# Optimization experiments

Measured on AMD Instinct MI355X. Metric: run time of the kernel, lower is better.

Reference implementation:

```python
import jax, jax.numpy as jnp
import numpy as np

B, N, D = 512, 16384, 2  # batch of weight vectors, grid points, 2-D geometry


def _eig_power(eigs, q, p):
    # reconstruct Q diag(eigs**p) Q^T ; eigs [B,D], q [B,D,D]
    return (q * (eigs ** p)[..., None, :]) @ jnp.swapaxes(q, -1, -2)


def _make_gauss(geo, w):
    # geo [N,D], w [B,N] (rows sum to 1)
    mean = w @ geo                               # [B,D]
    centered = geo[None, :, :] - mean[:, None, :]  # [B,N,D]
    denom = 1.0 - jnp.sum(w * w, axis=-1)        # [B] reliability-weight correction
    cov = jnp.einsum('bn,bnd,bne->bde', w, centered, centered) / denom[:, None, None]
    return mean, cov, centered


def setup_inputs() -> dict:
    key = jax.random.key(0)
    k1, k2, k3, k4 = jax.random.split(key, 4)
    geo_x = jax.random.uniform(k1, (N, D), dtype=jnp.float32)
    geo_y = jax.random.uniform(k2, (N, D), dtype=jnp.float32)
    a = jax.random.uniform(k3, (B, N), dtype=jnp.float32, minval=0.1, maxval=1.0)
    a = a / jnp.sum(a, axis=-1, keepdims=True)
    b = jax.random.uniform(k4, (B, N), dtype=jnp.float32, minval=0.1, maxval=1.0)
    b = b / jnp.sum(b, axis=-1, keepdims=True)
    return {"geo_x": geo_x, "geo_y": geo_y, "a": a, "b": b}


def reference(geo_x, geo_y, a, b):
    mean_a, cov_a, cx = _make_gauss(geo_x, a)   # cov_a [B,D,D], cx [B,N,D]
    mean_b, cov_b, _ = _make_gauss(geo_y, b)
    # Gaussian OT map: sigma0^{-1/2} (sigma0^{1/2} sigma1 sigma0^{1/2})^{1/2} sigma0^{-1/2}
    e0, q0 = jnp.linalg.eigh(cov_a)
    sqrt0 = _eig_power(e0, q0, 0.5)
    sqrt0_inv = _eig_power(e0, q0, -0.5)
    mid = sqrt0 @ cov_b @ sqrt0
    e1, q1 = jnp.linalg.eigh(mid)
    m = _eig_power(e1, q1, 0.5)
    a2b = sqrt0_inv @ m @ sqrt0_inv             # [B,D,D]
    # quadratic form (centered_x * (A2B centered_x^T)^T).sum(-1)
    quad = jnp.einsum('bnd,bde,bne->bn', cx, a2b, cx)  # [B,N]
    f = 2.0 * (0.5 * jnp.sum(geo_x * geo_x, axis=1)[None, :]
               - 0.5 * quad
               - mean_b @ geo_x.T)
    f = f - jnp.mean(f, axis=1, keepdims=True)
    return f
```

## Files before the change

### kernel.cpp

```cpp
#include <hip/hip_runtime.h>

static constexpr int TPB = 256;
static constexpr int NSLICE = 4;

using f4 = __attribute__((ext_vector_type(4))) float;

__device__ __forceinline__ float wave_reduce_f32(float v) {
#pragma unroll
    for (int off = 32; off > 0; off >>= 1)
        v += __shfl_down(v, off, 64);
    return v;
}

__global__ __launch_bounds__(TPB) void kstats(const float* __restrict__ gx,
                                              const float* __restrict__ gy,
                                              const float* __restrict__ a,
                                              const float* __restrict__ bw,
                                              int N, int B,
                                              double* __restrict__ spart,
                                              double* __restrict__ gpart) {
    const int s = blockIdx.x;
    const int b = blockIdx.y;
    const int n4   = N / 4;
    const int per  = n4 / NSLICE;
    const int base = s * per;
    const f4* gx4 = reinterpret_cast<const f4*>(gx);
    const int lane = threadIdx.x & 63, wid = threadIdx.x >> 6;

    if (b == B) {
        float sx = 0, sy = 0, sxx = 0, sxy = 0, syy = 0;
        for (int i = base + threadIdx.x; i < base + per; i += TPB) {
            f4 g0 = gx4[2 * i], g1 = gx4[2 * i + 1];
            float x0 = g0[0], y0 = g0[1], x1 = g0[2], y1 = g0[3];
            float x2 = g1[0], y2 = g1[1], x3 = g1[2], y3 = g1[3];
            sx  += (x0 + x1) + (x2 + x3);
            sy  += (y0 + y1) + (y2 + y3);
            sxx += x0 * x0 + x1 * x1 + x2 * x2 + x3 * x3;
            sxy += x0 * y0 + x1 * y1 + x2 * y2 + x3 * y3;
            syy += y0 * y0 + y1 * y1 + y2 * y2 + y3 * y3;
        }
        float accg[5] = {sx, sy, sxx, sxy, syy};
        __shared__ double redg[4][5];
#pragma unroll
        for (int k = 0; k < 5; k++) {
            float v = wave_reduce_f32(accg[k]);
            if (lane == 0) redg[wid][k] = (double)v;
        }
        __syncthreads();
        if (threadIdx.x < 5)
            gpart[s * 5 + threadIdx.x] = redg[0][threadIdx.x] + redg[1][threadIdx.x] +
                                         redg[2][threadIdx.x] + redg[3][threadIdx.x];
        return;
    }

    const f4* a4  = reinterpret_cast<const f4*>(a  + (size_t)b * N);
    const f4* b4  = reinterpret_cast<const f4*>(bw + (size_t)b * N);
    const f4* gy4 = reinterpret_cast<const f4*>(gy);

    float acc[12];
#pragma unroll
    for (int k = 0; k < 12; k++) acc[k] = 0.0f;

    const int i0 = base + threadIdx.x;

#pragma unroll
    for (int half = 0; half < 2; half++) {
        const int ia = i0 + (2 * half) * TPB;
        const int ib = i0 + (2 * half + 1) * TPB;
        f4 av0 = a4[ia],  av1 = a4[ib];
        f4 bv0 = b4[ia],  bv1 = b4[ib];
        f4 gA0 = gx4[2 * ia], gA1 = gx4[2 * ia + 1];
        f4 gB0 = gx4[2 * ib], gB1 = gx4[2 * ib + 1];
        f4 hA0 = gy4[2 * ia], hA1 = gy4[2 * ia + 1];
        f4 hB0 = gy4[2 * ib], hB1 = gy4[2 * ib + 1];

#pragma unroll
        for (int q = 0; q < 2; q++) {
            f4 av = q ? av1 : av0;
            f4 bv = q ? bv1 : bv0;
            f4 g0 = q ? gB0 : gA0, g1 = q ? gB1 : gA1;
            f4 h0 = q ? hB0 : hA0, h1 = q ? hB1 : hA1;
            float wa[4] = {av[0], av[1], av[2], av[3]};
            float wb[4] = {bv[0], bv[1], bv[2], bv[3]};
            float px[4] = {g0[0], g0[2], g1[0], g1[2]};
            float py[4] = {g0[1], g0[3], g1[1], g1[3]};
            float qx[4] = {h0[0], h0[2], h1[0], h1[2]};
            float qy[4] = {h0[1], h0[3], h1[1], h1[3]};
#pragma unroll
            for (int j = 0; j < 4; j++) {
                float w = wa[j], x = px[j], y = py[j];
                float wx = w * x, wy = w * y;
                acc[0] += wx;
                acc[1] += wy;
                acc[2] += wx * x;
                acc[3] += wx * y;
                acc[4] += wy * y;
                acc[5] += w * w;
                float v = wb[j], u = qx[j], t = qy[j];
                float vu = v * u, vt = v * t;
                acc[6]  += vu;
                acc[7]  += vt;
                acc[8]  += vu * u;
                acc[9]  += vu * t;
                acc[10] += vt * t;
                acc[11] += v * v;
            }
        }
    }

    __shared__ double red[4][12];
#pragma unroll
    for (int k = 0; k < 12; k++) {
        float v = wave_reduce_f32(acc[k]);
        if (lane == 0) red[wid][k] = (double)v;
    }
    __syncthreads();
    if (threadIdx.x < 12) {
        spart[((size_t)b * NSLICE + s) * 12 + threadIdx.x] =
            red[0][threadIdx.x] + red[1][threadIdx.x] +
            red[2][threadIdx.x] + red[3][threadIdx.x];
    }
}

__global__ __launch_bounds__(TPB) void kemit(const float* __restrict__ gx,
                                             const double* __restrict__ spart,
                                             const double* __restrict__ gpart,
                                             int N, float* __restrict__ out) {
    const int b = blockIdx.y;
    __shared__ double sh12[12];
    __shared__ double shg[5];
    __shared__ float shc[10];

    const f4* gx4 = reinterpret_cast<const f4*>(gx);
    const int i0 = blockIdx.x * (TPB * 4) + threadIdx.x;
    f4 g[8];
#pragma unroll
    for (int k = 0; k < 4; k++) {
        g[2 * k]     = gx4[2 * (i0 + k * TPB)];
        g[2 * k + 1] = gx4[2 * (i0 + k * TPB) + 1];
    }

    if (threadIdx.x < 12) {
        double t = 0;
#pragma unroll
        for (int s = 0; s < NSLICE; s++)
            t += spart[((size_t)b * NSLICE + s) * 12 + threadIdx.x];
        sh12[threadIdx.x] = t;
    } else if (threadIdx.x >= 64 && threadIdx.x < 69) {
        double t = 0;
#pragma unroll
        for (int s = 0; s < NSLICE; s++) t += gpart[s * 5 + (threadIdx.x - 64)];
        shg[threadIdx.x - 64] = t / (double)N;
    }
    __syncthreads();

    if (threadIdx.x == 0) {
        double mx  = sh12[0],  my  = sh12[1],  Saxx = sh12[2],  Saxy = sh12[3],  Sayy = sh12[4],  Saa = sh12[5];
        double mbx = sh12[6],  mby = sh12[7],  Sbxx = sh12[8],  Sbxy = sh12[9],  Sbyy = sh12[10], Sbb = sh12[11];

        double da = 1.0 - Saa, db = 1.0 - Sbb;
        double Caxx = (Saxx - mx * mx) / da;
        double Caxy = (Saxy - mx * my) / da;
        double Cayy = (Sayy - my * my) / da;
        double Cbxx = (Sbxx - mbx * mbx) / db;
        double Cbxy = (Sbxy - mbx * mby) / db;
        double Cbyy = (Sbyy - mby * mby) / db;

        double s0 = sqrt(fmax(Caxx * Cayy - Caxy * Caxy, 0.0));
        double t0 = sqrt(Caxx + Cayy + 2.0 * s0);
        double Rxx = (Caxx + s0) / t0, Rxy = Caxy / t0, Ryy = (Cayy + s0) / t0;
        double detR = Rxx * Ryy - Rxy * Rxy;
        double Ixx = Ryy / detR, Ixy = -Rxy / detR, Iyy = Rxx / detR;

        double Txx = Cbxx * Rxx + Cbxy * Rxy;
        double Txy = Cbxx * Rxy + Cbxy * Ryy;
        double Tyx = Cbxy * Rxx + Cbyy * Rxy;
        double Tyy = Cbxy * Rxy + Cbyy * Ryy;
        double midxx = Rxx * Txx + Rxy * Tyx;
        double midyy = Rxy * Txy + Ryy * Tyy;
        double midxy = 0.5 * ((Rxx * Txy + Rxy * Tyy) + (Rxy * Txx + Ryy * Tyx));

        double s1 = sqrt(fmax(midxx * midyy - midxy * midxy, 0.0));
        double t1 = sqrt(midxx + midyy + 2.0 * s1);
        double Mxx = (midxx + s1) / t1, Mxy = midxy / t1, Myy = (midyy + s1) / t1;

        double Uxx = Mxx * Ixx + Mxy * Ixy;
        double Uxy = Mxx * Ixy + Mxy * Iyy;
        double Uyx = Mxy * Ixx + Myy * Ixy;
        double Uyy = Mxy * Ixy + Myy * Iyy;
        double Axx = Ixx * Uxx + Ixy * Uyx;
        double Axy = Ixx * Uxy + Ixy * Uyy;
        double Ayy = Ixy * Uxy + Iyy * Uyy;

        shc[0] = (float)(1.0 - Axx);
        shc[1] = (float)(1.0 - Ayy);
        shc[2] = (float)(-2.0 * Axy);
        shc[3] = (float)(2.0 * (Axx * mx + Axy * my - mbx));
        shc[4] = (float)(2.0 * (Ayy * my + Axy * mx - mby));
        shc[5] = (float)shg[0];
        shc[6] = (float)shg[1];
        shc[7] = (float)shg[2];
        shc[8] = (float)shg[3];
        shc[9] = (float)shg[4];
    }
    __syncthreads();

    const float cxx = shc[0], cyy = shc[1], cxy = shc[2], cx = shc[3], cy = shc[4];
    const float Ex = shc[5], Ey = shc[6], Ex2 = shc[7], Exy = shc[8], Ey2 = shc[9];

    f4* out4 = reinterpret_cast<f4*>(out + (size_t)b * N);
#pragma unroll
    for (int k = 0; k < 4; k++) {
        int i = i0 + k * TPB;
        f4 g0 = g[2 * k], g1 = g[2 * k + 1];
        float rx[4] = {g0[0], g0[2], g1[0], g1[2]};
        float ry[4] = {g0[1], g0[3], g1[1], g1[3]};
        f4 o;
#pragma unroll
        for (int j = 0; j < 4; j++) {
            float x = rx[j], y = ry[j];
            o[j] = cxx * (x * x - Ex2) + cyy * (y * y - Ey2) + cxy * (x * y - Exy) +
                   cx * (x - Ex) + cy * (y - Ey);
        }
        __builtin_nontemporal_store(o, out4 + i);
    }
}

extern "C" void kernel_launch(void* const* d_in, const int* in_sizes, int n_in,
                              void* d_out, int out_size, void* d_ws, size_t ws_size,
                              hipStream_t stream) {
    const float* geo_x = (const float*)d_in[0];
    const float* geo_y = (const float*)d_in[1];
    const float* a     = (const float*)d_in[2];
    const float* b     = (const float*)d_in[3];
    float* out = (float*)d_out;

    int N = in_sizes[0] / 2;
    int B = in_sizes[2] / N;

    char* ws = (char*)d_ws;
    double* gpart = (double*)ws;
    double* spart = (double*)(ws + 512);

    kstats<<<dim3(NSLICE, B + 1), TPB, 0, stream>>>(geo_x, geo_y, a, b, N, B,
                                                    spart, gpart);
    kemit<<<dim3((N / 4) / (TPB * 4), B), TPB, 0, stream>>>(geo_x, spart, gpart, N, out);
}
```

Measured before the change: 26.14 us.

## Batch eight rows per emit block and fold mean-centering into a constant

The emit kernel now has each block handle eight batch rows over a smaller point slice. It loads the geometry once and reuses it for every row, and eight threads compute the per-row 2x2 OT coefficients in parallel instead of one. The mean-subtraction terms are folded into a single constant K, so the per-point polynomial becomes a short FMA chain. The stats kernel also issues all four loads up front instead of two at a time. Fewer blocks and more work per block cut redundant geometry reads and serial setup, but reduce grid parallelism and assume B is divisible by eight.

Result: slower. 27.21 us (+4.1%).

```diff
diff --git a/kernel.cpp b/kernel.cpp
--- a/kernel.cpp
+++ b/kernel.cpp
@@ -2,6 +2,8 @@
 
 static constexpr int TPB = 256;
 static constexpr int NSLICE = 4;
+static constexpr int ROWB = 8;
+static constexpr int PF = 2;
 
 using f4 = __attribute__((ext_vector_type(4))) float;
 
@@ -62,49 +64,44 @@
     for (int k = 0; k < 12; k++) acc[k] = 0.0f;
 
     const int i0 = base + threadIdx.x;
-
-#pragma unroll
-    for (int half = 0; half < 2; half++) {
-        const int ia = i0 + (2 * half) * TPB;
-        const int ib = i0 + (2 * half + 1) * TPB;
-        f4 av0 = a4[ia],  av1 = a4[ib];
-        f4 bv0 = b4[ia],  bv1 = b4[ib];
-        f4 gA0 = gx4[2 * ia], gA1 = gx4[2 * ia + 1];
-        f4 gB0 = gx4[2 * ib], gB1 = gx4[2 * ib + 1];
-        f4 hA0 = gy4[2 * ia], hA1 = gy4[2 * ia + 1];
-        f4 hB0 = gy4[2 * ib], hB1 = gy4[2 * ib + 1];
-
-#pragma unroll
-        for (int q = 0; q < 2; q++) {
-            f4 av = q ? av1 : av0;
-            f4 bv = q ? bv1 : bv0;
-            f4 g0 = q ? gB0 : gA0, g1 = q ? gB1 : gA1;
-            f4 h0 = q ? hB0 : hA0, h1 = q ? hB1 : hA1;
-            float wa[4] = {av[0], av[1], av[2], av[3]};
-            float wb[4] = {bv[0], bv[1], bv[2], bv[3]};
-            float px[4] = {g0[0], g0[2], g1[0], g1[2]};
-            float py[4] = {g0[1], g0[3], g1[1], g1[3]};
-            float qx[4] = {h0[0], h0[2], h1[0], h1[2]};
-            float qy[4] = {h0[1], h0[3], h1[1], h1[3]};
-#pragma unroll
-            for (int j = 0; j < 4; j++) {
-                float w = wa[j], x = px[j], y = py[j];
-                float wx = w * x, wy = w * y;
-                acc[0] += wx;
-                acc[1] += wy;
-                acc[2] += wx * x;
-                acc[3] += wx * y;
-                acc[4] += wy * y;
-                acc[5] += w * w;
-                float v = wb[j], u = qx[j], t = qy[j];
-                float vu = v * u, vt = v * t;
-                acc[6]  += vu;
-                acc[7]  += vt;
-                acc[8]  += vu * u;
-                acc[9]  += vu * t;
-                acc[10] += vt * t;
-                acc[11] += v * v;
-            }
+    f4 av[4], bv[4], gA[4], gB[4], hA[4], hB[4];
+#pragma unroll
+    for (int q = 0; q < 4; q++) {
+        const int i = i0 + q * TPB;
+        av[q] = a4[i];
+        bv[q] = b4[i];
+        gA[q] = gx4[2 * i];
+        gB[q] = gx4[2 * i + 1];
+        hA[q] = gy4[2 * i];
+        hB[q] = gy4[2 * i + 1];
+    }
+
+#pragma unroll
+    for (int q = 0; q < 4; q++) {
+        float wa[4] = {av[q][0], av[q][1], av[q][2], av[q][3]};
+        float wb[4] = {bv[q][0], bv[q][1], bv[q][2], bv[q][3]};
+        float px[4] = {gA[q][0], gA[q][2], gB[q][0], gB[q][2]};
+        float py[4] = {gA[q][1], gA[q][3], gB[q][1], gB[q][3]};
+        float qx[4] = {hA[q][0], hA[q][2], hB[q][0], hB[q][2]};
+        float qy[4] = {hA[q][1], hA[q][3], hB[q][1], hB[q][3]};
+#pragma unroll
+        for (int j = 0; j < 4; j++) {
+            float w = wa[j], x = px[j], y = py[j];
+            float wx = w * x, wy = w * y;
+            acc[0] += wx;
+            acc[1] += wy;
+            acc[2] += wx * x;
+            acc[3] += wx * y;
+            acc[4] += wy * y;
+            acc[5] += w * w;
+            float v = wb[j], u = qx[j], t = qy[j];
+            float vu = v * u, vt = v * t;
+            acc[6]  += vu;
+            acc[7]  += vt;
+            acc[8]  += vu * u;
+            acc[9]  += vu * t;
+            acc[10] += vt * t;
+            acc[11] += v * v;
         }
     }
 
@@ -126,37 +123,40 @@
                                              const double* __restrict__ spart,
                                              const double* __restrict__ gpart,
                                              int N, float* __restrict__ out) {
-    const int b = blockIdx.y;
-    __shared__ double sh12[12];
-    __shared__ double shg[5];
-    __shared__ float shc[10];
+    const int b0 = blockIdx.y * ROWB;
+    __shared__ float shc[ROWB][8];
 
     const f4* gx4 = reinterpret_cast<const f4*>(gx);
-    const int i0 = blockIdx.x * (TPB * 4) + threadIdx.x;
-    f4 g[8];
-#pragma unroll
-    for (int k = 0; k < 4; k++) {
+    const int i0 = blockIdx.x * (TPB * PF) + threadIdx.x;
+    f4 g[2 * PF];
+#pragma unroll
+    for (int k = 0; k < PF; k++) {
         g[2 * k]     = gx4[2 * (i0 + k * TPB)];
         g[2 * k + 1] = gx4[2 * (i0 + k * TPB) + 1];
     }
 
-    if (threadIdx.x < 12) {
-        double t = 0;
-#pragma unroll
-        for (int s = 0; s < NSLICE; s++)
-            t += spart[((size_t)b * NSLICE + s) * 12 + threadIdx.x];
-        sh12[threadIdx.x] = t;
-    } else if (threadIdx.x >= 64 && threadIdx.x < 69) {
-        double t = 0;
-#pragma unroll
-        for (int s = 0; s < NSLICE; s++) t += gpart[s * 5 + (threadIdx.x - 64)];
-        shg[threadIdx.x - 64] = t / (double)N;
-    }
-    __syncthreads();
-
-    if (threadIdx.x == 0) {
-        double mx  = sh12[0],  my  = sh12[1],  Saxx = sh12[2],  Saxy = sh12[3],  Sayy = sh12[4],  Saa = sh12[5];
-        double mbx = sh12[6],  mby = sh12[7],  Sbxx = sh12[8],  Sbxy = sh12[9],  Sbyy = sh12[10], Sbb = sh12[11];
+    if (threadIdx.x < ROWB) {
+        const int r = b0 + threadIdx.x;
+        double s12[12];
+#pragma unroll
+        for (int k = 0; k < 12; k++) {
+            double t = 0;
+#pragma unroll
+            for (int s = 0; s < NSLICE; s++)
+                t += spart[((size_t)r * NSLICE + s) * 12 + k];
+            s12[k] = t;
+        }
+        double gm[5];
+#pragma unroll
+        for (int k = 0; k < 5; k++) {
+            double t = 0;
+#pragma unroll
+            for (int s = 0; s < NSLICE; s++) t += gpart[s * 5 + k];
+            gm[k] = t / (double)N;
+        }
+
+        double mx  = s12[0],  my  = s12[1],  Saxx = s12[2],  Saxy = s12[3],  Sayy = s12[4],  Saa = s12[5];
+        double mbx = s12[6],  mby = s12[7],  Sbxx = s12[8],  Sbxy = s12[9],  Sbyy = s12[10], Sbb = s12[11];
 
         double da = 1.0 - Saa, db = 1.0 - Sbb;
         double Caxx = (Saxx - mx * mx) / da;
@@ -192,37 +192,43 @@
         double Axy = Ixx * Uxy + Ixy * Uyy;
         double Ayy = Ixy * Uxy + Iyy * Uyy;
 
-        shc[0] = (float)(1.0 - Axx);
-        shc[1] = (float)(1.0 - Ayy);
-        shc[2] = (float)(-2.0 * Axy);
-        shc[3] = (float)(2.0 * (Axx * mx + Axy * my - mbx));
-        shc[4] = (float)(2.0 * (Ayy * my + Axy * mx - mby));
-        shc[5] = (float)shg[0];
-        shc[6] = (float)shg[1];
-        shc[7] = (float)shg[2];
-        shc[8] = (float)shg[3];
-        shc[9] = (float)shg[4];
+        double cxx = 1.0 - Axx;
+        double cyy = 1.0 - Ayy;
+        double cxy = -2.0 * Axy;
+        double cx  = 2.0 * (Axx * mx + Axy * my - mbx);
+        double cy  = 2.0 * (Ayy * my + Axy * mx - mby);
+        double K   = cxx * gm[2] + cyy * gm[4] + cxy * gm[3] + cx * gm[0] + cy * gm[1];
+        shc[threadIdx.x][0] = (float)cxx;
+        shc[threadIdx.x][1] = (float)cyy;
+        shc[threadIdx.x][2] = (float)cxy;
+        shc[threadIdx.x][3] = (float)cx;
+        shc[threadIdx.x][4] = (float)cy;
+        shc[threadIdx.x][5] = (float)K;
     }
     __syncthreads();
 
-    const float cxx = shc[0], cyy = shc[1], cxy = shc[2], cx = shc[3], cy = shc[4];
-    const float Ex = shc[5], Ey = shc[6], Ex2 = shc[7], Exy = shc[8], Ey2 = shc[9];
-
-    f4* out4 = reinterpret_cast<f4*>(out + (size_t)b * N);
-#pragma unroll
-    for (int k = 0; k < 4; k++) {
-        int i = i0 + k * TPB;
-        f4 g0 = g[2 * k], g1 = g[2 * k + 1];
-        float rx[4] = {g0[0], g0[2], g1[0], g1[2]};
-        float ry[4] = {g0[1], g0[3], g1[1], g1[3]};
-        f4 o;
-#pragma unroll
-        for (int j = 0; j < 4; j++) {
-            float x = rx[j], y = ry[j];
-            o[j] = cxx * (x * x - Ex2) + cyy * (y * y - Ey2) + cxy * (x * y - Exy) +
-                   cx * (x - Ex) + cy * (y - Ey);
-        }
-        __builtin_nontemporal_store(o, out4 + i);
+#pragma unroll
+    for (int r = 0; r < ROWB; r++) {
+        const float cxx = shc[r][0], cyy = shc[r][1], cxy = shc[r][2];
+        const float cx = shc[r][3], cy = shc[r][4], K = shc[r][5];
+        f4* out4 = reinterpret_cast<f4*>(out + (size_t)(b0 + r) * N);
+#pragma unroll
+        for (int k = 0; k < PF; k++) {
+            f4 g0 = g[2 * k], g1 = g[2 * k + 1];
+            float rx[4] = {g0[0], g0[2], g1[0], g1[2]};
+            float ry[4] = {g0[1], g0[3], g1[1], g1[3]};
+            f4 o;
+#pragma unroll
+            for (int j = 0; j < 4; j++) {
+                float x = rx[j], y = ry[j];
+                float t1v = fmaf(cyy, y, cy);
+                float t2v = fmaf(y, t1v, -K);
+                float t3v = fmaf(cxx, x, cx);
+                float t4v = fmaf(cxy, y, t3v);
+                o[j] = fmaf(x, t4v, t2v);
+            }
+            __builtin_nontemporal_store(o, out4 + (i0 + k * TPB));
+        }
     }
 }
 
@@ -244,5 +250,6 @@
 
     kstats<<<dim3(NSLICE, B + 1), TPB, 0, stream>>>(geo_x, geo_y, a, b, N, B,
                                                     spart, gpart);
-    kemit<<<dim3((N / 4) / (TPB * 4), B), TPB, 0, stream>>>(geo_x, spart, gpart, N, out);
-}
+    kemit<<<dim3((N / 4) / (TPB * PF), B / ROWB), TPB, 0, stream>>>(geo_x, spart,
+                                                                    gpart, N, out);
+}
```
